# Kernel optimization log

Hardware: AMD Instinct MI355X
Metric: run time of the kernel (lower is better)

Reference implementation:

```python
import jax, jax.numpy as jnp
import numpy as np

N = 100000   # nodes
E = 3200000  # edges (avg degree 32)
D = 512      # dim_latent
NEG_SLOPE = 0.01  # nn.LeakyReLU default


def setup_inputs() -> dict:
    key = jax.random.key(0)
    ks = jax.random.split(key, 14)
    weight = jax.random.normal(ks[0], (N,), dtype=jnp.float32)
    significance = jax.random.randint(ks[1], (N,), 0, 2, dtype=jnp.int32)
    src = jax.random.randint(ks[2], (E,), 0, N, dtype=jnp.int32)
    dst = jax.random.randint(ks[3], (E,), 0, N, dtype=jnp.int32)
    emb_table = jax.random.normal(ks[4], (2, 2), dtype=jnp.float32)
    lin_W = jax.random.normal(ks[5], (3, D), dtype=jnp.float32) / np.sqrt(3.0)
    lin_b = jnp.zeros((D,), dtype=jnp.float32)
    s = 1.0 / np.sqrt(D)
    W0 = jax.random.normal(ks[6], (D, D), dtype=jnp.float32) * s
    b0 = jnp.zeros((D,), dtype=jnp.float32)
    W1 = jax.random.normal(ks[7], (D, D), dtype=jnp.float32) * s
    b1 = jnp.zeros((D,), dtype=jnp.float32)
    W2 = jax.random.normal(ks[8], (D, D), dtype=jnp.float32) * s
    b2 = jnp.zeros((D,), dtype=jnp.float32)
    pred_W = jax.random.normal(ks[9], (D, 1), dtype=jnp.float32) * s
    pred_b = jnp.zeros((1,), dtype=jnp.float32)
    return {"weight": weight, "significance": significance, "src": src, "dst": dst,
            "emb_table": emb_table, "lin_W": lin_W, "lin_b": lin_b,
            "W0": W0, "b0": b0, "W1": W1, "b1": b1, "W2": W2, "b2": b2,
            "pred_W": pred_W, "pred_b": pred_b}


def _gcn_layer(feat, src, dst, n_out, n_in, W, b):
    # DGL GraphConv norm='both' with self-loops already folded into degrees.
    h = feat * n_out[:, None]                                   # [N, D] src-normalize
    agg = jax.ops.segment_sum(h[src], dst, num_segments=N)      # SpMM aggregate
    agg = agg + h                                               # self-loop message
    agg = agg * n_in[:, None]                                   # dst-normalize
    return agg @ W + b


def reference(weight, significance, src, dst, emb_table, lin_W, lin_b,
              W0, b0, W1, b1, W2, b2, pred_W, pred_b):
    ones = jnp.ones((E,), dtype=jnp.float32)
    deg_out = jax.ops.segment_sum(ones, src, num_segments=N) + 1.0  # +1 self-loop
    deg_in = jax.ops.segment_sum(ones, dst, num_segments=N) + 1.0
    n_out = jax.lax.rsqrt(deg_out)
    n_in = jax.lax.rsqrt(deg_in)

    sig = emb_table[significance]                            # [N, 2]
    feats = jnp.concatenate([weight[:, None], sig], axis=1)  # [N, 3]
    feats = feats @ lin_W + lin_b                            # [N, D]

    h = _gcn_layer(feats, src, dst, n_out, n_in, W0, b0)
    for W, b in ((W1, b1), (W2, b2)):
        h = jnp.where(h >= 0, h, NEG_SLOPE * h)              # LeakyReLU
        h = _gcn_layer(h, src, dst, n_out, n_in, W, b)

    # NOTE: original forward's `if self.train:` is always truthy (method object),
    # so it always returns the prediction logits.
    logits = h @ pred_W + pred_b                             # [N, 1]
    return logits
```

## Files before the change

### kernel.cpp

```cpp
#include <hip/hip_runtime.h>

#define N_NODES 100000
#define M_PAD 100096
#define N_EDGES 3200000
#define DIM 512
#define SLOTS 80
#define NEG_SLOPE 0.01f

#define B_PRE 12500
#define B_WT (B_PRE + 2048)
#define B_WP (B_WT + 129)
#define B_FEAT (B_WP + 25000)

typedef _Float16 f16;
typedef _Float16 f16x8 __attribute__((ext_vector_type(8)));
typedef float f32x4 __attribute__((ext_vector_type(4)));

__device__ __forceinline__ void load_lds16(const void* g, void* l) {
  __builtin_amdgcn_global_load_lds(
      (const __attribute__((address_space(1))) void*)g,
      (__attribute__((address_space(3))) void*)l, 16, 0, 0);
}

__global__ void k_setup(const int* __restrict__ src, const int* __restrict__ dst,
                        int* __restrict__ cnt_o, int* __restrict__ cnt_i,
                        int* __restrict__ ell,
                        const float* __restrict__ W0, const float* __restrict__ W1,
                        f16* __restrict__ Wt,
                        const float* __restrict__ W2, const float* __restrict__ b2,
                        const float* __restrict__ pW, const float* __restrict__ pb,
                        float* __restrict__ wt_vec, float* __restrict__ c_out,
                        const float* __restrict__ weight, const int* __restrict__ sig,
                        const float* __restrict__ emb, const float* __restrict__ linW,
                        const float* __restrict__ linb, f16* __restrict__ Xs) {
  const int bid = blockIdx.x;
  const int tid = threadIdx.x;
  if (bid < B_PRE) {
    int e = bid * 256 + tid;
    int s = src[e];
    atomicAdd(&cnt_o[s], 1);
    int d = dst[e];
    int p = atomicAdd(&cnt_i[d], 1);
    if (p < SLOTS) ell[(size_t)d * SLOTS + p] = s;
  } else if (bid < B_WT) {
    int idx = (bid - B_PRE) * 256 + tid;
    int l = idx >> 18;
    int r = idx & 262143;
    int n = r >> 9, k = r & 511;
    const float* W = l ? W1 : W0;
    Wt[idx] = (f16)W[k * DIM + n];
  } else if (bid < B_WP) {
    int wid = tid >> 6, lane = tid & 63;
    int t = (bid - B_WT) * 4 + wid;
    if (t < DIM) {
      float s = 0.f;
#pragma unroll
      for (int n = 0; n < DIM; n += 64) s += W2[t * DIM + n + lane] * pW[n + lane];
#pragma unroll
      for (int off = 32; off; off >>= 1) s += __shfl_down(s, off, 64);
      if (lane == 0) wt_vec[t] = s;
    } else if (t == DIM) {
      float s = 0.f;
#pragma unroll
      for (int n = 0; n < DIM; n += 64) s += b2[n + lane] * pW[n + lane];
#pragma unroll
      for (int off = 32; off; off >>= 1) s += __shfl_down(s, off, 64);
      if (lane == 0) c_out[0] = s + pb[0];
    }
  } else {
    int wid = tid >> 6, lane = tid & 63;
    int node = (bid - B_WP) * 4 + wid;
    float w = weight[node];
    int sg = sig[node];
    float s0 = emb[sg * 2], s1 = emb[sg * 2 + 1];
    int d0 = lane * 8;
    f16x8 v;
#pragma unroll
    for (int k = 0; k < 8; k++) {
      int d = d0 + k;
      v[k] = (f16)(w * linW[d] + s0 * linW[DIM + d] + s1 * linW[2 * DIM + d] + linb[d]);
    }
    *(f16x8*)(Xs + (size_t)node * DIM + d0) = v;
  }
}

__global__ void k_norms(const int* __restrict__ cnt_o, const int* __restrict__ cnt_i,
                        float* __restrict__ n_out, float* __restrict__ n_in) {
  int i = blockIdx.x * blockDim.x + threadIdx.x;
  if (i < N_NODES) {
    n_out[i] = rsqrtf((float)cnt_o[i] + 1.0f);
    n_in[i] = rsqrtf((float)cnt_i[i] + 1.0f);
  }
}


__global__ void k_spmm(const f16* __restrict__ Xs, f16* __restrict__ A,
                       const int* __restrict__ ell, const int* __restrict__ cnt_i,
                       const float* __restrict__ n_in, const float* __restrict__ n_out) {
  int wid = threadIdx.x >> 6, lane = threadIdx.x & 63;
  int node = blockIdx.x * 4 + wid;
  int d0 = lane * 8;
  float acc[8];
  {
    f16x8 v = *(const f16x8*)(Xs + (size_t)node * DIM + d0);
    float no = n_out[node];
#pragma unroll
    for (int k = 0; k < 8; k++) acc[k] = no * (float)v[k];
  }
  int deg = cnt_i[node];
  if (deg > SLOTS) deg = SLOTS;
  const int* erow = ell + (size_t)node * SLOTS;
  const f16* base = Xs + d0;
  int j = 0;
  for (; j + 8 <= deg; j += 8) {
    int ix[8];
#pragma unroll
    for (int u = 0; u < 8; u++) ix[u] = erow[j + u];
    float sc[8];
#pragma unroll
    for (int u = 0; u < 8; u++) sc[u] = n_out[ix[u]];
    f16x8 v[8];
#pragma unroll
    for (int u = 0; u < 8; u++) v[u] = *(const f16x8*)(base + (size_t)ix[u] * DIM);
#pragma unroll
    for (int u = 0; u < 8; u++)
#pragma unroll
      for (int k = 0; k < 8; k++) acc[k] += sc[u] * (float)v[u][k];
  }
  for (; j < deg; ++j) {
    int sn = erow[j];
    float sc = n_out[sn];
    f16x8 v = *(const f16x8*)(base + (size_t)sn * DIM);
#pragma unroll
    for (int k = 0; k < 8; k++) acc[k] += sc * (float)v[k];
  }
  float ni = n_in[node];
  f16x8 o;
#pragma unroll
  for (int k = 0; k < 8; k++) o[k] = (f16)(acc[k] * ni);
  __builtin_nontemporal_store(o, (f16x8*)(A + (size_t)node * DIM + d0));
}

__global__ __launch_bounds__(256) void k_gemm(const f16* __restrict__ A, const f16* __restrict__ Wt,
                                              const float* __restrict__ bias,
                                              const float* __restrict__ n_out,
                                              f16* __restrict__ Y,
                                              const float* __restrict__ wt_vec,
                                              float* __restrict__ yv) {
  __shared__ __align__(1024) char smem[32768];
  __shared__ float yred[128];
  const int tid = threadIdx.x;
  const int wid = tid >> 6, lane = tid & 63;
  const int lr = lane & 15, lk = lane >> 4;
  const int wr = wid >> 1, wc = wid & 1;
  const int cb = blockIdx.x * 128;
  const int rb = blockIdx.y * 128;
  const int ls = lane >> 3;
  const int ss = lane & 7;

  f32x4 acc[4][4];
#pragma unroll
  for (int i = 0; i < 4; i++)
#pragma unroll
    for (int j = 0; j < 4; j++) acc[i][j] = (f32x4){0.f, 0.f, 0.f, 0.f};

  for (int kb = 0; kb < DIM; kb += 64) {
#pragma unroll
    for (int i = 0; i < 4; i++) {
      int c = wid * 4 + i;
      int r = c * 8 + ls;
      int goff = (ss * 16) ^ ((r & 7) << 4);
      const char* ga = (const char*)A + ((size_t)(rb + r) * DIM + kb) * 2 + goff;
      load_lds16(ga, smem + c * 1024);
      const char* gw = (const char*)Wt + ((size_t)(cb + r) * DIM + kb) * 2 + goff;
      load_lds16(gw, smem + 16384 + c * 1024);
    }
    __syncthreads();
#pragma unroll
    for (int kk = 0; kk < 2; kk++) {
      f16x8 a[4], b[4];
#pragma unroll
      for (int fm = 0; fm < 4; fm++) {
        int row = wr * 64 + fm * 16 + lr;
        int byt = row * 128 + ((kk * 64 + lk * 16) ^ ((row & 7) << 4));
        a[fm] = *(const f16x8*)(smem + byt);
      }
#pragma unroll
      for (int fn = 0; fn < 4; fn++) {
        int row = wc * 64 + fn * 16 + lr;
        int byt = row * 128 + ((kk * 64 + lk * 16) ^ ((row & 7) << 4));
        b[fn] = *(const f16x8*)(smem + 16384 + byt);
      }
#pragma unroll
      for (int fm = 0; fm < 4; fm++)
#pragma unroll
        for (int fn = 0; fn < 4; fn++)
          acc[fm][fn] = __builtin_amdgcn_mfma_f32_16x16x32_f16(a[fm], b[fn], acc[fm][fn], 0, 0, 0);
    }
    __syncthreads();
  }

  if (yv == nullptr) {
#pragma unroll
    for (int fn = 0; fn < 4; fn++) {
      int col = cb + wc * 64 + fn * 16 + lr;
      float bv = bias[col];
#pragma unroll
      for (int fm = 0; fm < 4; fm++) {
#pragma unroll
        for (int r = 0; r < 4; r++) {
          int row = rb + wr * 64 + fm * 16 + lk * 4 + r;
          if (row < N_NODES) {
            float v = acc[fm][fn][r] + bv;
            v = (v >= 0.f) ? v : NEG_SLOPE * v;
            Y[(size_t)row * DIM + col] = (f16)v;
          }
        }
      }
    }
  } else {
    if (tid < 128) yred[tid] = 0.f;
    __syncthreads();
#pragma unroll
    for (int fm = 0; fm < 4; fm++) {
#pragma unroll
      for (int r = 0; r < 4; r++) {
        int rloc = wr * 64 + fm * 16 + lk * 4 + r;
        int row = rb + rloc;
        float p = 0.f;
#pragma unroll
        for (int fn = 0; fn < 4; fn++) {
          int col = cb + wc * 64 + fn * 16 + lr;
          float v = acc[fm][fn][r] + bias[col];
          v = (v >= 0.f) ? v : NEG_SLOPE * v;
          p += v * wt_vec[col];
        }
        if (row < N_NODES) atomicAdd(&yred[rloc], p * n_out[row]);
      }
    }
    __syncthreads();
    if (tid < 128) {
      int row = rb + tid;
      if (row < N_NODES) atomicAdd(&yv[row], yred[tid]);
    }
  }
}

__global__ void k_sagg(const float* __restrict__ y, const int* __restrict__ ell,
                       const int* __restrict__ cnt_i, const float* __restrict__ n_in,
                       const float* __restrict__ c_out, float* __restrict__ out) {
  int i = blockIdx.x * blockDim.x + threadIdx.x;
  if (i >= N_NODES) return;
  int deg = cnt_i[i];
  if (deg > SLOTS) deg = SLOTS;
  const int* erow = ell + (size_t)i * SLOTS;
  float s = y[i];
  int j = 0;
  for (; j + 8 <= deg; j += 8) {
    int4 a = *(const int4*)(erow + j);
    int4 b = *(const int4*)(erow + j + 4);
    s += y[a.x] + y[a.y] + y[a.z] + y[a.w];
    s += y[b.x] + y[b.y] + y[b.z] + y[b.w];
  }
  for (; j < deg; ++j) s += y[erow[j]];
  out[i] = n_in[i] * s + c_out[0];
}

extern "C" void kernel_launch(void* const* d_in, const int* in_sizes, int n_in_cnt,
                              void* d_out, int out_size, void* d_ws, size_t ws_size,
                              hipStream_t stream) {
  const float* weight = (const float*)d_in[0];
  const int* sig = (const int*)d_in[1];
  const int* src = (const int*)d_in[2];
  const int* dst = (const int*)d_in[3];
  const float* emb = (const float*)d_in[4];
  const float* linW = (const float*)d_in[5];
  const float* linb = (const float*)d_in[6];
  const float* W0 = (const float*)d_in[7];
  const float* b0 = (const float*)d_in[8];
  const float* W1 = (const float*)d_in[9];
  const float* b1 = (const float*)d_in[10];
  const float* W2 = (const float*)d_in[11];
  const float* b2 = (const float*)d_in[12];
  const float* pW = (const float*)d_in[13];
  const float* pb = (const float*)d_in[14];
  float* out = (float*)d_out;

  char* ws = (char*)d_ws;
  size_t off = 0;
  auto alloc = [&](size_t bytes) {
    void* p = ws + off;
    off += (bytes + 255) & ~(size_t)255;
    return p;
  };
  int* cnt_o = (int*)alloc((size_t)N_NODES * 4);
  int* cnt_i = (int*)alloc((size_t)N_NODES * 4);
  float* yv = (float*)alloc((size_t)N_NODES * 4);
  float* n_out = (float*)alloc((size_t)N_NODES * 4);
  float* n_in = (float*)alloc((size_t)N_NODES * 4);
  int* ell = (int*)alloc((size_t)N_NODES * SLOTS * 4);
  f16* Wt = (f16*)alloc((size_t)2 * DIM * DIM * 2);
  float* wt_vec = (float*)alloc((size_t)DIM * 4);
  float* c_out = (float*)alloc(256);
  f16* B0 = (f16*)alloc((size_t)M_PAD * DIM * 2);
  f16* B1 = (f16*)alloc((size_t)M_PAD * DIM * 2);

  dim3 blk(256);
  hipMemsetAsync(cnt_o, 0, (char*)n_out - (char*)cnt_o, stream);
  k_setup<<<B_FEAT, blk, 0, stream>>>(src, dst, cnt_o, cnt_i, ell,
                                      W0, W1, Wt, W2, b2, pW, pb, wt_vec, c_out,
                                      weight, sig, emb, linW, linb, B0);
  k_norms<<<(N_NODES + 255) / 256, blk, 0, stream>>>(cnt_o, cnt_i, n_out, n_in);

  dim3 ggrid(DIM / 128, M_PAD / 128);
  k_spmm<<<N_NODES / 4, blk, 0, stream>>>(B0, B1, ell, cnt_i, n_in, n_out);
  k_gemm<<<ggrid, blk, 0, stream>>>(B1, Wt, b0, n_out, B0, nullptr, nullptr);
  k_spmm<<<N_NODES / 4, blk, 0, stream>>>(B0, B1, ell, cnt_i, n_in, n_out);
  k_gemm<<<ggrid, blk, 0, stream>>>(B1, Wt + (size_t)DIM * DIM, b1, n_out, nullptr, wt_vec, yv);
  k_sagg<<<(N_NODES + 255) / 256, blk, 0, stream>>>(yv, ell, cnt_i, n_in, c_out, out);
}
```

Before: 1.640 ms.

## Overlap SpMM of second half with GEMM of first half in mixed kernel

Measured after the change: 1.644 ms. About the same (+0.2%).

```diff
diff --git a/kernel.cpp b/kernel.cpp
--- a/kernel.cpp
+++ b/kernel.cpp
@@ -6,6 +6,10 @@
 #define DIM 512
 #define SLOTS 80
 #define NEG_SLOPE 0.01f
+#define HROW 50048
+#define HTIL 391
+#define NB_H0 12512
+#define NB_H1 12488
 
 #define B_PRE 12500
 #define B_WT (B_PRE + 2048)
@@ -94,45 +98,71 @@
 }
 
 
-__global__ void k_spmm(const f16* __restrict__ Xs, f16* __restrict__ A,
-                       const int* __restrict__ ell, const int* __restrict__ cnt_i,
-                       const float* __restrict__ n_in, const float* __restrict__ n_out) {
-  int wid = threadIdx.x >> 6, lane = threadIdx.x & 63;
-  int node = blockIdx.x * 4 + wid;
+__device__ __forceinline__ void spmm_body(const f16* __restrict__ Xlo,
+                                          const f16* __restrict__ Xhi, int H,
+                                          f16* __restrict__ A,
+                                          const int* __restrict__ ell,
+                                          const int* __restrict__ cnt_i,
+                                          const float* __restrict__ n_in,
+                                          const float* __restrict__ n_out,
+                                          int node, int lane) {
   int d0 = lane * 8;
   float acc[8];
   {
-    f16x8 v = *(const f16x8*)(Xs + (size_t)node * DIM + d0);
-    float no = n_out[node];
-#pragma unroll
-    for (int k = 0; k < 8; k++) acc[k] = no * (float)v[k];
+    const f16* sb = (node < H ? Xlo : Xhi) + (size_t)node * DIM + d0;
+    f16x8 v = *(const f16x8*)sb;
+    float ss = n_out ? n_out[node] : 1.f;
+#pragma unroll
+    for (int k = 0; k < 8; k++) acc[k] = ss * (float)v[k];
   }
   int deg = cnt_i[node];
   if (deg > SLOTS) deg = SLOTS;
   const int* erow = ell + (size_t)node * SLOTS;
-  const f16* base = Xs + d0;
   int j = 0;
-  for (; j + 8 <= deg; j += 8) {
-    int ix[8];
-#pragma unroll
-    for (int u = 0; u < 8; u++) ix[u] = erow[j + u];
-    float sc[8];
-#pragma unroll
-    for (int u = 0; u < 8; u++) sc[u] = n_out[ix[u]];
-    f16x8 v[8];
-#pragma unroll
-    for (int u = 0; u < 8; u++) v[u] = *(const f16x8*)(base + (size_t)ix[u] * DIM);
-#pragma unroll
-    for (int u = 0; u < 8; u++)
-#pragma unroll
-      for (int k = 0; k < 8; k++) acc[k] += sc[u] * (float)v[u][k];
-  }
-  for (; j < deg; ++j) {
-    int sn = erow[j];
-    float sc = n_out[sn];
-    f16x8 v = *(const f16x8*)(base + (size_t)sn * DIM);
-#pragma unroll
-    for (int k = 0; k < 8; k++) acc[k] += sc * (float)v[k];
+  if (n_out) {
+    for (; j + 8 <= deg; j += 8) {
+      int ix[8];
+#pragma unroll
+      for (int u = 0; u < 8; u++) ix[u] = erow[j + u];
+      float sc[8];
+#pragma unroll
+      for (int u = 0; u < 8; u++) sc[u] = n_out[ix[u]];
+      f16x8 v[8];
+#pragma unroll
+      for (int u = 0; u < 8; u++)
+        v[u] = *(const f16x8*)((ix[u] < H ? Xlo : Xhi) + (size_t)ix[u] * DIM + d0);
+#pragma unroll
+      for (int u = 0; u < 8; u++)
+#pragma unroll
+        for (int k = 0; k < 8; k++) acc[k] += sc[u] * (float)v[u][k];
+    }
+    for (; j < deg; ++j) {
+      int sn = erow[j];
+      float sc = n_out[sn];
+      f16x8 v = *(const f16x8*)((sn < H ? Xlo : Xhi) + (size_t)sn * DIM + d0);
+#pragma unroll
+      for (int k = 0; k < 8; k++) acc[k] += sc * (float)v[k];
+    }
+  } else {
+    for (; j + 8 <= deg; j += 8) {
+      int ix[8];
+#pragma unroll
+      for (int u = 0; u < 8; u++) ix[u] = erow[j + u];
+      f16x8 v[8];
+#pragma unroll
+      for (int u = 0; u < 8; u++)
+        v[u] = *(const f16x8*)((ix[u] < H ? Xlo : Xhi) + (size_t)ix[u] * DIM + d0);
+#pragma unroll
+      for (int u = 0; u < 8; u++)
+#pragma unroll
+        for (int k = 0; k < 8; k++) acc[k] += (float)v[u][k];
+    }
+    for (; j < deg; ++j) {
+      int sn = erow[j];
+      f16x8 v = *(const f16x8*)((sn < H ? Xlo : Xhi) + (size_t)sn * DIM + d0);
+#pragma unroll
+      for (int k = 0; k < 8; k++) acc[k] += (float)v[k];
+    }
   }
   float ni = n_in[node];
   f16x8 o;
@@ -141,20 +171,20 @@
   __builtin_nontemporal_store(o, (f16x8*)(A + (size_t)node * DIM + d0));
 }
 
-__global__ __launch_bounds__(256) void k_gemm(const f16* __restrict__ A, const f16* __restrict__ Wt,
-                                              const float* __restrict__ bias,
-                                              const float* __restrict__ n_out,
-                                              f16* __restrict__ Y,
-                                              const float* __restrict__ wt_vec,
-                                              float* __restrict__ yv) {
-  __shared__ __align__(1024) char smem[32768];
-  __shared__ float yred[128];
-  const int tid = threadIdx.x;
+__device__ __forceinline__ void gemm_body(char* smem, float* yred,
+                                          const f16* __restrict__ A,
+                                          const f16* __restrict__ Wt,
+                                          const float* __restrict__ bias,
+                                          const float* __restrict__ n_out,
+                                          f16* __restrict__ Y,
+                                          const float* __restrict__ wt_vec,
+                                          float* __restrict__ yv,
+                                          int bx, int by, int tid) {
   const int wid = tid >> 6, lane = tid & 63;
   const int lr = lane & 15, lk = lane >> 4;
   const int wr = wid >> 1, wc = wid & 1;
-  const int cb = blockIdx.x * 128;
-  const int rb = blockIdx.y * 128;
+  const int cb = bx * 128;
+  const int rb = by * 128;
   const int ls = lane >> 3;
   const int ss = lane & 7;
 
@@ -213,6 +243,7 @@
           if (row < N_NODES) {
             float v = acc[fm][fn][r] + bv;
             v = (v >= 0.f) ? v : NEG_SLOPE * v;
+            v *= n_out[row];
             Y[(size_t)row * DIM + col] = (f16)v;
           }
         }
@@ -235,7 +266,7 @@
           v = (v >= 0.f) ? v : NEG_SLOPE * v;
           p += v * wt_vec[col];
         }
-        if (row < N_NODES) atomicAdd(&yred[rloc], p * n_out[row]);
+        if (row < N_NODES) atomicAdd(&yred[rloc & 127], p * n_out[row]);
       }
     }
     __syncthreads();
@@ -243,6 +274,58 @@
       int row = rb + tid;
       if (row < N_NODES) atomicAdd(&yv[row], yred[tid]);
     }
+  }
+}
+
+
+__global__ void k_spmm(const f16* __restrict__ Xlo, const f16* __restrict__ Xhi, int H,
+                       f16* __restrict__ A, const int* __restrict__ ell,
+                       const int* __restrict__ cnt_i, const float* __restrict__ n_in,
+                       const float* __restrict__ n_out, int node0) {
+  int wid = threadIdx.x >> 6, lane = threadIdx.x & 63;
+  int node = node0 + blockIdx.x * 4 + wid;
+  if (node >= N_NODES) return;
+  spmm_body(Xlo, Xhi, H, A, ell, cnt_i, n_in, n_out, node, lane);
+}
+
+__global__ __launch_bounds__(256) void k_gemm(const f16* __restrict__ A, const f16* __restrict__ Wt,
+                                              const float* __restrict__ bias,
+                                              const float* __restrict__ n_out,
+                                              f16* __restrict__ Y,
+                                              const float* __restrict__ wt_vec,
+                                              float* __restrict__ yv, int tile_off) {
+  __shared__ __align__(1024) char smem[32768];
+  __shared__ float yred[128];
+  gemm_body(smem, yred, A, Wt, bias, n_out, Y, wt_vec, yv,
+            blockIdx.x, blockIdx.y + tile_off, threadIdx.x);
+}
+
+__global__ __launch_bounds__(256) void k_mix(const f16* __restrict__ Xlo,
+                                             const f16* __restrict__ Xhi, int H,
+                                             f16* __restrict__ A,
+                                             const int* __restrict__ ell,
+                                             const int* __restrict__ cnt_i,
+                                             const float* __restrict__ n_in,
+                                             const float* __restrict__ n_out_spmm,
+                                             const f16* __restrict__ Ag,
+                                             const f16* __restrict__ Wt,
+                                             const float* __restrict__ bias,
+                                             const float* __restrict__ n_out,
+                                             f16* __restrict__ Y,
+                                             const float* __restrict__ wt_vec,
+                                             float* __restrict__ yv,
+                                             int G4, int node0) {
+  __shared__ __align__(1024) char smem[32768];
+  __shared__ float yred[128];
+  const int bid = blockIdx.x;
+  if (bid < G4) {
+    gemm_body(smem, yred, Ag, Wt, bias, n_out, Y, wt_vec, yv,
+              bid & 3, bid >> 2, threadIdx.x);
+  } else {
+    int wid = threadIdx.x >> 6, lane = threadIdx.x & 63;
+    int node = node0 + (bid - G4) * 4 + wid;
+    if (node >= N_NODES) return;
+    spmm_body(Xlo, Xhi, H, A, ell, cnt_i, n_in, n_out_spmm, node, lane);
   }
 }
 
@@ -304,6 +387,9 @@
   float* c_out = (float*)alloc(256);
   f16* B0 = (f16*)alloc((size_t)M_PAD * DIM * 2);
   f16* B1 = (f16*)alloc((size_t)M_PAD * DIM * 2);
+  size_t base_end = off;
+  f16* SP = (f16*)alloc((size_t)HROW * DIM * 2);
+  bool overlap = (off <= ws_size);
 
   dim3 blk(256);
   hipMemsetAsync(cnt_o, 0, (char*)n_out - (char*)cnt_o, stream);
@@ -312,10 +398,28 @@
                                       weight, sig, emb, linW, linb, B0);
   k_norms<<<(N_NODES + 255) / 256, blk, 0, stream>>>(cnt_o, cnt_i, n_out, n_in);
 
-  dim3 ggrid(DIM / 128, M_PAD / 128);
-  k_spmm<<<N_NODES / 4, blk, 0, stream>>>(B0, B1, ell, cnt_i, n_in, n_out);
-  k_gemm<<<ggrid, blk, 0, stream>>>(B1, Wt, b0, n_out, B0, nullptr, nullptr);
-  k_spmm<<<N_NODES / 4, blk, 0, stream>>>(B0, B1, ell, cnt_i, n_in, n_out);
-  k_gemm<<<ggrid, blk, 0, stream>>>(B1, Wt + (size_t)DIM * DIM, b1, n_out, nullptr, wt_vec, yv);
+  if (overlap) {
+    const int G4 = HTIL * 4;
+    k_spmm<<<NB_H0, blk, 0, stream>>>(B0, B0, HROW, B1, ell, cnt_i, n_in, n_out, 0);
+    k_mix<<<G4 + NB_H1, blk, 0, stream>>>(B0, B0, HROW, B1, ell, cnt_i, n_in, n_out,
+                                          B1, Wt, b0, n_out, SP, nullptr, nullptr,
+                                          G4, HROW);
+    dim3 gg(4, HTIL);
+    k_gemm<<<gg, blk, 0, stream>>>(B1, Wt, b0, n_out, B0, nullptr, nullptr, HTIL);
+    k_spmm<<<NB_H0, blk, 0, stream>>>(SP, B0, HROW, B1, ell, cnt_i, n_in, nullptr, 0);
+    k_mix<<<G4 + NB_H1, blk, 0, stream>>>(SP, B0, HROW, B1, ell, cnt_i, n_in, nullptr,
+                                          B1, Wt + (size_t)DIM * DIM, b1, n_out,
+                                          nullptr, wt_vec, yv, G4, HROW);
+    k_gemm<<<gg, blk, 0, stream>>>(B1, Wt + (size_t)DIM * DIM, b1, n_out, nullptr,
+                                   wt_vec, yv, HTIL);
+  } else {
+    (void)base_end;
+    dim3 gfull(4, M_PAD / 128);
+    k_spmm<<<25000, blk, 0, stream>>>(B0, B0, HROW, B1, ell, cnt_i, n_in, n_out, 0);
+    k_gemm<<<gfull, blk, 0, stream>>>(B1, Wt, b0, n_out, B0, nullptr, nullptr, 0);
+    k_spmm<<<25000, blk, 0, stream>>>(B0, B0, HROW, B1, ell, cnt_i, n_in, nullptr, 0);
+    k_gemm<<<gfull, blk, 0, stream>>>(B1, Wt + (size_t)DIM * DIM, b1, n_out, nullptr,
+                                      wt_vec, yv, 0);
+  }
   k_sagg<<<(N_NODES + 255) / 256, blk, 0, stream>>>(yv, ell, cnt_i, n_in, c_out, out);
 }
```

## Privatize out-degree atomics and fold src-normalization into GEMM epilogue

Applied to the files above, without the earlier changes.

Measured after the change: 1.635 ms. No clear change (-0.3%).

```diff
diff --git a/kernel.cpp b/kernel.cpp
--- a/kernel.cpp
+++ b/kernel.cpp
@@ -23,8 +23,8 @@
 }
 
 __global__ void k_setup(const int* __restrict__ src, const int* __restrict__ dst,
-                        int* __restrict__ cnt_o, int* __restrict__ cnt_i,
-                        int* __restrict__ ell,
+                        int* __restrict__ cnt_op, int pmask,
+                        int* __restrict__ cnt_i, int* __restrict__ ell,
                         const float* __restrict__ W0, const float* __restrict__ W1,
                         f16* __restrict__ Wt,
                         const float* __restrict__ W2, const float* __restrict__ b2,
@@ -38,7 +38,7 @@
   if (bid < B_PRE) {
     int e = bid * 256 + tid;
     int s = src[e];
-    atomicAdd(&cnt_o[s], 1);
+    atomicAdd(&cnt_op[(size_t)(bid & pmask) * N_NODES + s], 1);
     int d = dst[e];
     int p = atomicAdd(&cnt_i[d], 1);
     if (p < SLOTS) ell[(size_t)d * SLOTS + p] = s;
@@ -84,11 +84,14 @@
   }
 }
 
-__global__ void k_norms(const int* __restrict__ cnt_o, const int* __restrict__ cnt_i,
+__global__ void k_norms(const int* __restrict__ cnt_op, int nparts,
+                        const int* __restrict__ cnt_i,
                         float* __restrict__ n_out, float* __restrict__ n_in) {
   int i = blockIdx.x * blockDim.x + threadIdx.x;
   if (i < N_NODES) {
-    n_out[i] = rsqrtf((float)cnt_o[i] + 1.0f);
+    int d = 0;
+    for (int p = 0; p < nparts; p++) d += cnt_op[(size_t)p * N_NODES + i];
+    n_out[i] = rsqrtf((float)d + 1.0f);
     n_in[i] = rsqrtf((float)cnt_i[i] + 1.0f);
   }
 }
@@ -103,36 +106,57 @@
   float acc[8];
   {
     f16x8 v = *(const f16x8*)(Xs + (size_t)node * DIM + d0);
-    float no = n_out[node];
-#pragma unroll
-    for (int k = 0; k < 8; k++) acc[k] = no * (float)v[k];
+    float ss = n_out ? n_out[node] : 1.f;
+#pragma unroll
+    for (int k = 0; k < 8; k++) acc[k] = ss * (float)v[k];
   }
   int deg = cnt_i[node];
   if (deg > SLOTS) deg = SLOTS;
   const int* erow = ell + (size_t)node * SLOTS;
   const f16* base = Xs + d0;
   int j = 0;
-  for (; j + 8 <= deg; j += 8) {
-    int ix[8];
-#pragma unroll
-    for (int u = 0; u < 8; u++) ix[u] = erow[j + u];
-    float sc[8];
-#pragma unroll
-    for (int u = 0; u < 8; u++) sc[u] = n_out[ix[u]];
-    f16x8 v[8];
-#pragma unroll
-    for (int u = 0; u < 8; u++) v[u] = *(const f16x8*)(base + (size_t)ix[u] * DIM);
-#pragma unroll
-    for (int u = 0; u < 8; u++)
-#pragma unroll
-      for (int k = 0; k < 8; k++) acc[k] += sc[u] * (float)v[u][k];
-  }
-  for (; j < deg; ++j) {
-    int sn = erow[j];
-    float sc = n_out[sn];
-    f16x8 v = *(const f16x8*)(base + (size_t)sn * DIM);
-#pragma unroll
-    for (int k = 0; k < 8; k++) acc[k] += sc * (float)v[k];
+  if (n_out) {
+    for (; j + 8 <= deg; j += 8) {
+      int ix[8];
+#pragma unroll
+      for (int u = 0; u < 8; u++) ix[u] = erow[j + u];
+      float sc[8];
+#pragma unroll
+      for (int u = 0; u < 8; u++) sc[u] = n_out[ix[u]];
+      f16x8 v[8];
+#pragma unroll
+      for (int u = 0; u < 8; u++) v[u] = *(const f16x8*)(base + (size_t)ix[u] * DIM);
+#pragma unroll
+      for (int u = 0; u < 8; u++)
+#pragma unroll
+        for (int k = 0; k < 8; k++) acc[k] += sc[u] * (float)v[u][k];
+    }
+    for (; j < deg; ++j) {
+      int sn = erow[j];
+      float sc = n_out[sn];
+      f16x8 v = *(const f16x8*)(base + (size_t)sn * DIM);
+#pragma unroll
+      for (int k = 0; k < 8; k++) acc[k] += sc * (float)v[k];
+    }
+  } else {
+    for (; j + 8 <= deg; j += 8) {
+      int ix[8];
+#pragma unroll
+      for (int u = 0; u < 8; u++) ix[u] = erow[j + u];
+      f16x8 v[8];
+#pragma unroll
+      for (int u = 0; u < 8; u++) v[u] = *(const f16x8*)(base + (size_t)ix[u] * DIM);
+#pragma unroll
+      for (int u = 0; u < 8; u++)
+#pragma unroll
+        for (int k = 0; k < 8; k++) acc[k] += (float)v[u][k];
+    }
+    for (; j < deg; ++j) {
+      int sn = erow[j];
+      f16x8 v = *(const f16x8*)(base + (size_t)sn * DIM);
+#pragma unroll
+      for (int k = 0; k < 8; k++) acc[k] += (float)v[k];
+    }
   }
   float ni = n_in[node];
   f16x8 o;
@@ -213,6 +237,7 @@
           if (row < N_NODES) {
             float v = acc[fm][fn][r] + bv;
             v = (v >= 0.f) ? v : NEG_SLOPE * v;
+            v *= n_out[row];
             Y[(size_t)row * DIM + col] = (f16)v;
           }
         }
@@ -293,7 +318,6 @@
     off += (bytes + 255) & ~(size_t)255;
     return p;
   };
-  int* cnt_o = (int*)alloc((size_t)N_NODES * 4);
   int* cnt_i = (int*)alloc((size_t)N_NODES * 4);
   float* yv = (float*)alloc((size_t)N_NODES * 4);
   float* n_out = (float*)alloc((size_t)N_NODES * 4);
@@ -305,17 +329,23 @@
   f16* B0 = (f16*)alloc((size_t)M_PAD * DIM * 2);
   f16* B1 = (f16*)alloc((size_t)M_PAD * DIM * 2);
 
+  size_t avail = (ws_size > off) ? (ws_size - off) : 0;
+  int P = (int)(avail / ((size_t)N_NODES * 4));
+  P = (P >= 16) ? 16 : (P >= 8) ? 8 : (P >= 4) ? 4 : (P >= 2) ? 2 : 1;
+  int* cnt_op = (int*)(ws + off);
+
   dim3 blk(256);
-  hipMemsetAsync(cnt_o, 0, (char*)n_out - (char*)cnt_o, stream);
-  k_setup<<<B_FEAT, blk, 0, stream>>>(src, dst, cnt_o, cnt_i, ell,
+  hipMemsetAsync(cnt_i, 0, (char*)n_out - (char*)cnt_i, stream);
+  hipMemsetAsync(cnt_op, 0, (size_t)P * N_NODES * 4, stream);
+  k_setup<<<B_FEAT, blk, 0, stream>>>(src, dst, cnt_op, P - 1, cnt_i, ell,
                                       W0, W1, Wt, W2, b2, pW, pb, wt_vec, c_out,
                                       weight, sig, emb, linW, linb, B0);
-  k_norms<<<(N_NODES + 255) / 256, blk, 0, stream>>>(cnt_o, cnt_i, n_out, n_in);
+  k_norms<<<(N_NODES + 255) / 256, blk, 0, stream>>>(cnt_op, P, cnt_i, n_out, n_in);
 
   dim3 ggrid(DIM / 128, M_PAD / 128);
   k_spmm<<<N_NODES / 4, blk, 0, stream>>>(B0, B1, ell, cnt_i, n_in, n_out);
   k_gemm<<<ggrid, blk, 0, stream>>>(B1, Wt, b0, n_out, B0, nullptr, nullptr);
-  k_spmm<<<N_NODES / 4, blk, 0, stream>>>(B0, B1, ell, cnt_i, n_in, n_out);
+  k_spmm<<<N_NODES / 4, blk, 0, stream>>>(B0, B1, ell, cnt_i, n_in, nullptr);
   k_gemm<<<ggrid, blk, 0, stream>>>(B1, Wt + (size_t)DIM * DIM, b1, n_out, nullptr, wt_vec, yv);
   k_sagg<<<(N_NODES + 255) / 256, blk, 0, stream>>>(yv, ell, cnt_i, n_in, c_out, out);
 }
```
